# Kernel optimization log

Hardware: AMD Instinct MI355X
Metric: run time of the kernel (lower is better)

Reference implementation:

```python
import jax, jax.numpy as jnp
import numpy as np

EPS = 1e-5

def _face_normals(v, vi):
    # v: [B,V,3], vi: [F,3] -> [B,F,3]
    pts = v[:, vi]                                  # [B,F,3,3]
    n = jnp.cross(pts[:, :, 1] - pts[:, :, 0], pts[:, :, 2] - pts[:, :, 0])
    norm = jnp.linalg.norm(n, axis=-1, keepdims=True)
    return n / jnp.where(norm < EPS, 1.0, norm)

def _vert_normals(v, vi):
    fn = _face_normals(v, vi)                       # [B,F,3]
    fn_rep = jnp.repeat(fn, 3, axis=1)              # [B,3F,3] (one copy per face vertex)
    vn = jnp.zeros_like(v).at[:, vi.reshape(-1)].add(fn_rep)
    norm = jnp.linalg.norm(vn, axis=-1, keepdims=True)
    return vn / jnp.where(norm < EPS, 1.0, norm)

def _values_to_uv(values, index_image, bary_image):
    # values: [B,V,C]; index_image/bary_image: [U,U,3] -> [B,C,U,U]
    mask = jnp.all(index_image != -1, axis=-1)      # [U,U]
    idx = jnp.clip(index_image, 0, values.shape[1] - 1)
    vals = values[:, idx]                           # [B,U,U,3,C]
    uv = jnp.einsum('buvkc,uvk->bcuv', vals, bary_image.astype(values.dtype))
    return uv * mask[None, None].astype(values.dtype)

def _grid_sample_bilinear(img, gx, gy):
    # img: [B,C,H,W]; gx,gy: [N] in [-1,1]; align_corners=False, zero padding
    B, C, H, W = img.shape
    ix = ((gx + 1.0) * W - 1.0) * 0.5
    iy = ((gy + 1.0) * H - 1.0) * 0.5
    x0 = jnp.floor(ix); y0 = jnp.floor(iy)
    x1 = x0 + 1.0;      y1 = y0 + 1.0
    wx1 = ix - x0; wx0 = 1.0 - wx1
    wy1 = iy - y0; wy0 = 1.0 - wy1
    def gather(xi, yi):
        valid = (xi >= 0) & (xi < W) & (yi >= 0) & (yi < H)
        xc = jnp.clip(xi, 0, W - 1).astype(jnp.int32)
        yc = jnp.clip(yi, 0, H - 1).astype(jnp.int32)
        return img[:, :, yc, xc] * valid.astype(img.dtype)  # [B,C,N]
    return (gather(x0, y0) * (wx0 * wy0) + gather(x1, y0) * (wx1 * wy0)
          + gather(x0, y1) * (wx0 * wy1) + gather(x1, y1) * (wx1 * wy1))

def _sample_uv(values_uv, uv_coords, v2uv):
    g = uv_coords * 2.0 - 1.0                       # [T,2]
    vals = _grid_sample_bilinear(values_uv, g[:, 0], g[:, 1])  # [B,C,T]
    vals = jnp.transpose(vals, (0, 2, 1))           # [B,T,C]
    return vals[:, v2uv].mean(axis=2)               # [B,V,C]

def setup_inputs() -> dict:
    key = jax.random.key(0)
    ks = jax.random.split(key, 6)
    B, V, Fc, U, T, K = 8, 100000, 200000, 1024, 110000, 2
    verts = jax.random.normal(ks[0], (B, V, 3), jnp.float32)
    vi = jax.random.randint(ks[1], (Fc, 3), 0, V, dtype=jnp.int32)
    index_image = jax.random.randint(ks[2], (U, U, 3), 0, V, dtype=jnp.int32)
    bary_image = jax.random.uniform(ks[3], (U, U, 3), jnp.float32)
    vt = jax.random.uniform(ks[4], (T, 2), jnp.float32)
    v2uv = jax.random.randint(ks[5], (V, K), 0, T, dtype=jnp.int32)
    return {"verts": verts, "bary_image": bary_image, "vt": vt,
            "vi": vi, "index_image": index_image, "v2uv": v2uv}

def reference(verts, bary_image, vt, vi, index_image, v2uv):
    vn = _vert_normals(verts, vi)                   # [B,V,3]
    uv = _values_to_uv(vn, index_image, bary_image) # [B,3,U,U]
    return _sample_uv(uv, vt, v2uv)                 # [B,V,3]
```

## Files before the change

kernel.cpp:

```cpp
#include <hip/hip_runtime.h>
#include <hip/hip_fp16.h>

#define EPS 1e-5f

constexpr int B = 8;
constexpr int V = 100000;
constexpr int F = 200000;
constexpr int U = 1024;
constexpr int T = 110000;
constexpr int CAP = 24;

constexpr int NBUK = (V + 127) / 128;
constexpr int N4   = (3 * F) / 4;
constexpr int EB   = (N4 + 255) / 256;
constexpr int TRB  = (V + 255) / 256;

constexpr int FQ   = 8;
constexpr int FNB  = (F * 8 / FQ + 255) / 256;
constexpr int TQ   = 4;
constexpr int CPB  = (T / TQ + 255) / 256;
constexpr int SQ   = 2;
constexpr int VQ   = 2;

struct alignas(8) h4 { __half2 a, b; };
__device__ inline h4 pack_h4(float x, float y, float z) {
    h4 r; r.a = __floats2half2_rn(x, y); r.b = __floats2half2_rn(z, 0.0f);
    return r;
}
__device__ inline float3 unpack_h4(h4 v) {
    float2 xy = __half22float2(v.a);
    float2 zw = __half22float2(v.b);
    return make_float3(xy.x, xy.y, zw.x);
}

struct alignas(16) Corner16 { unsigned lo, hi; __half2 w01; __half2 w2_; };
__device__ inline Corner16 pack_corner(int i0, int i1, int i2,
                                       float w0, float w1, float w2) {
    unsigned long long x = (unsigned long long)(unsigned)i0
                         | ((unsigned long long)(unsigned)i1 << 21)
                         | ((unsigned long long)(unsigned)i2 << 42);
    Corner16 c;
    c.lo = (unsigned)x;
    c.hi = (unsigned)(x >> 32);
    c.w01 = __floats2half2_rn(w0, w1);
    c.w2_ = __floats2half2_rn(w2, 0.0f);
    return c;
}

__global__ void k1_pre(const float* __restrict__ verts,
                       float* __restrict__ vertsT,
                       const int* __restrict__ vi,
                       int* __restrict__ tot,
                       const int* __restrict__ index_image,
                       const float* __restrict__ bary_image,
                       const float* __restrict__ vt,
                       Corner16* __restrict__ corners) {
    __shared__ int lh[NBUK];
    int blk = blockIdx.x;

    if (blk < TRB) {
        int v = blk * 256 + threadIdx.x;
        if (v >= V) return;
        float buf[24];
#pragma unroll
        for (int b = 0; b < 8; ++b) {
            const float* p = verts + (size_t)b * V * 3 + (size_t)v * 3;
            buf[b * 3 + 0] = p[0];
            buf[b * 3 + 1] = p[1];
            buf[b * 3 + 2] = p[2];
        }
        float4* dst = (float4*)(vertsT + (size_t)v * 24);
#pragma unroll
        for (int i = 0; i < 6; ++i)
            dst[i] = make_float4(buf[4 * i], buf[4 * i + 1],
                                 buf[4 * i + 2], buf[4 * i + 3]);
        return;
    }

    if (blk < TRB + EB) {
        int k = blk - TRB;
        for (int i = threadIdx.x; i < NBUK; i += 256) lh[i] = 0;
        __syncthreads();
        int m4 = k * 256 + threadIdx.x;
        if (m4 < N4) {
            int4 e = ((const int4*)vi)[m4];
            atomicAdd(&lh[e.x >> 7], 1);
            atomicAdd(&lh[e.y >> 7], 1);
            atomicAdd(&lh[e.z >> 7], 1);
            atomicAdd(&lh[e.w >> 7], 1);
        }
        __syncthreads();
        for (int b = threadIdx.x; b < NBUK; b += 256)
            if (lh[b]) atomicAdd(&tot[b], lh[b]);
        return;
    }

    int tbase = (blk - TRB - EB) * 256 + threadIdx.x;
    if (tbase >= T / TQ) return;
#pragma unroll
    for (int qq = 0; qq < TQ; ++qq) {
        int t = tbase + qq * (T / TQ);

        float gx = vt[t * 2 + 0];
        float gy = vt[t * 2 + 1];
        float ix = gx * (float)U - 0.5f;
        float iy = gy * (float)U - 0.5f;

        float x0f = floorf(ix);
        float y0f = floorf(iy);
        int x0 = (int)x0f;
        int y0 = (int)y0f;
        float wx1 = ix - x0f, wx0 = 1.0f - wx1;
        float wy1 = iy - y0f, wy0 = 1.0f - wy1;

#pragma unroll
        for (int c = 0; c < 4; ++c) {
            int cy = c >> 1, cx = c & 1;
            int y = y0 + cy;
            int x = x0 + cx;
            int i0 = 0, i1 = 0, i2 = 0;
            float w0 = 0.0f, w1 = 0.0f, w2 = 0.0f;
            if (x >= 0 && x < U && y >= 0 && y < U) {
                float w = (cy ? wy1 : wy0) * (cx ? wx1 : wx0);
                int pix = y * U + x;
                int j0 = index_image[pix * 3 + 0];
                int j1 = index_image[pix * 3 + 1];
                int j2 = index_image[pix * 3 + 2];
                float m = (j0 != -1 && j1 != -1 && j2 != -1) ? 1.0f : 0.0f;
                float wm = w * m;
                i0 = min(max(j0, 0), V - 1);
                i1 = min(max(j1, 0), V - 1);
                i2 = min(max(j2, 0), V - 1);
                w0 = wm * bary_image[pix * 3 + 0];
                w1 = wm * bary_image[pix * 3 + 1];
                w2 = wm * bary_image[pix * 3 + 2];
            }
            corners[t * 4 + c] = pack_corner(i0, i1, i2, w0, w1, w2);
        }
    }
}

__device__ inline void scan_base(const int* __restrict__ tot,
                                 int* pre, int* part) {
    constexpr int CH = (NBUK + 255) / 256;
    int th = threadIdx.x;
    int loc[CH];
    int local = 0;
#pragma unroll
    for (int j = 0; j < CH; ++j) {
        int idx = th * CH + j;
        int c = (idx < NBUK) ? tot[idx] : 0;
        loc[j] = local;
        local += c;
    }
    part[th] = local;
    __syncthreads();
    for (int off = 1; off < 256; off <<= 1) {
        int x = (th >= off) ? part[th - off] : 0;
        __syncthreads();
        part[th] += x;
        __syncthreads();
    }
    int excl = part[th] - local;
#pragma unroll
    for (int j = 0; j < CH; ++j) {
        int idx = th * CH + j;
        if (idx < NBUK) pre[idx] = excl + loc[j];
    }
    if (th == 255) pre[NBUK] = part[255];
    __syncthreads();
}

__global__ __launch_bounds__(256, 2) void k2_fused(
        const int* __restrict__ vi,
        const float* __restrict__ vertsT,
        h4* __restrict__ fn,
        const int* __restrict__ tot,
        int* __restrict__ cursor,
        int* __restrict__ pairs) {
    int blk = blockIdx.x;

    if (blk < FNB) {
        int id = blk * 256 + threadIdx.x;
        if (id >= F * 8 / FQ) return;
        int b = id & 7;
        int fbase = id >> 3;
        const float3* vT = (const float3*)vertsT;

        int ia[FQ], ib[FQ], ic[FQ];
        float3 p0[FQ], p1[FQ], p2[FQ];
#pragma unroll
        for (int q = 0; q < FQ; ++q) {
            int f = fbase + q * (F / FQ);
            ia[q] = vi[f * 3 + 0];
            ib[q] = vi[f * 3 + 1];
            ic[q] = vi[f * 3 + 2];
        }
#pragma unroll
        for (int q = 0; q < FQ; ++q) {
            p0[q] = vT[(size_t)ia[q] * 8 + b];
            p1[q] = vT[(size_t)ib[q] * 8 + b];
            p2[q] = vT[(size_t)ic[q] * 8 + b];
        }
#pragma unroll
        for (int q = 0; q < FQ; ++q) {
            int f = fbase + q * (F / FQ);
            float e1x = p1[q].x - p0[q].x, e1y = p1[q].y - p0[q].y, e1z = p1[q].z - p0[q].z;
            float e2x = p2[q].x - p0[q].x, e2y = p2[q].y - p0[q].y, e2z = p2[q].z - p0[q].z;

            float nx = e1y * e2z - e1z * e2y;
            float ny = e1z * e2x - e1x * e2z;
            float nz = e1x * e2y - e1y * e2x;

            float norm = sqrtf(nx * nx + ny * ny + nz * nz);
            float inv = (norm < EPS) ? 1.0f : (1.0f / norm);
            fn[(size_t)f * 8 + b] = pack_h4(nx * inv, ny * inv, nz * inv);
        }
        return;
    }

    __shared__ int pre[NBUK + 1];
    __shared__ int part[256];
    __shared__ int lh[NBUK];
    __shared__ int base[NBUK];
    scan_base(tot, pre, part);
    for (int i = threadIdx.x; i < NBUK; i += 256) lh[i] = 0;
    __syncthreads();

    int k = blk - FNB;
    int m4 = k * 256 + threadIdx.x;
    bool act = (m4 < N4);
    int vv[4], rr[4], bbk[4], fc[4];
    if (act) {
        int4 e = ((const int4*)vi)[m4];
        vv[0] = e.x; vv[1] = e.y; vv[2] = e.z; vv[3] = e.w;
        int be = m4 * 4;
#pragma unroll
        for (int j = 0; j < 4; ++j) {
            bbk[j] = vv[j] >> 7;
            rr[j] = atomicAdd(&lh[bbk[j]], 1);
            fc[j] = (be + j) / 3;
        }
    }
    __syncthreads();
    for (int i = threadIdx.x; i < NBUK; i += 256)
        base[i] = lh[i] ? atomicAdd(&cursor[i], lh[i]) : 0;
    __syncthreads();
    if (act) {
#pragma unroll
        for (int j = 0; j < 4; ++j) {
            int pos = pre[bbk[j]] + base[bbk[j]] + rr[j];
            pairs[pos] = ((vv[j] & 127) << 18) | fc[j];
        }
    }
}

__global__ __launch_bounds__(256) void k5_gather(
        const int* __restrict__ pairs,
        const int* __restrict__ tot,
        const h4* __restrict__ fn,
        h4* __restrict__ vn) {
    __shared__ int cnt[128];
    __shared__ int rows[128 * CAP];
    __shared__ int pre[NBUK + 1];
    __shared__ int part[256];
    scan_base(tot, pre, part);

    int tid = threadIdx.x;
    if (tid < 128) cnt[tid] = 0;
    __syncthreads();

    int b = blockIdx.x;
    int start = pre[b], end = pre[b + 1];
    for (int i = start + tid; i < end; i += 256) {
        int pk = pairs[i];
        int vl = pk >> 18;
        int f = pk & 0x3FFFF;
        int pos = atomicAdd(&cnt[vl], 1);
        if (pos < CAP) rows[vl * CAP + pos] = f;
    }
    __syncthreads();

    int v0 = b << 7;
    for (int id = tid; id < 128 * 8; id += 256) {
        int vl = id >> 3, b8 = id & 7;
        int v = v0 + vl;
        if (v >= V) continue;
        int deg = min(cnt[vl], CAP);
        float ax = 0.0f, ay = 0.0f, az = 0.0f;
        int j = 0;
        for (; j + 1 < deg; j += 2) {
            h4 r0 = fn[(size_t)rows[vl * CAP + j] * 8 + b8];
            h4 r1 = fn[(size_t)rows[vl * CAP + j + 1] * 8 + b8];
            float3 n0 = unpack_h4(r0);
            float3 n1 = unpack_h4(r1);
            ax += n0.x + n1.x; ay += n0.y + n1.y; az += n0.z + n1.z;
        }
        if (j < deg) {
            float3 n = unpack_h4(fn[(size_t)rows[vl * CAP + j] * 8 + b8]);
            ax += n.x; ay += n.y; az += n.z;
        }
        float nn = sqrtf(ax * ax + ay * ay + az * az);
        float inv = (nn < EPS) ? 1.0f : (1.0f / nn);
        vn[(size_t)v * 8 + b8] = pack_h4(ax * inv, ay * inv, az * inv);
    }
}

__global__ void sample_points(const h4* __restrict__ vn,
                              const Corner16* __restrict__ corners,
                              h4* __restrict__ vals) {
    int id = blockIdx.x * blockDim.x + threadIdx.x;
    if (id >= (T / SQ) * 8) return;
    int b = id & 7;
    int tb = id >> 3;

#pragma unroll
    for (int s = 0; s < SQ; ++s) {
        int t = tb + s * (T / SQ);
        float ax = 0.0f, ay = 0.0f, az = 0.0f;
        Corner16 cr[4];
#pragma unroll
        for (int c = 0; c < 4; ++c) cr[c] = corners[t * 4 + c];
        h4 q[12];
#pragma unroll
        for (int c = 0; c < 4; ++c) {
            unsigned long long x = (unsigned long long)cr[c].lo
                                 | ((unsigned long long)cr[c].hi << 32);
            int i0 = (int)(x & 0x1FFFFF);
            int i1 = (int)((x >> 21) & 0x1FFFFF);
            int i2 = (int)(x >> 42);
            q[c * 3 + 0] = vn[(size_t)i0 * 8 + b];
            q[c * 3 + 1] = vn[(size_t)i1 * 8 + b];
            q[c * 3 + 2] = vn[(size_t)i2 * 8 + b];
        }
#pragma unroll
        for (int c = 0; c < 4; ++c) {
            float2 w01 = __half22float2(cr[c].w01);
            float w2 = __low2float(cr[c].w2_);
            float3 q0 = unpack_h4(q[c * 3 + 0]);
            float3 q1 = unpack_h4(q[c * 3 + 1]);
            float3 q2 = unpack_h4(q[c * 3 + 2]);
            ax += w01.x * q0.x + w01.y * q1.x + w2 * q2.x;
            ay += w01.x * q0.y + w01.y * q1.y + w2 * q2.y;
            az += w01.x * q0.z + w01.y * q1.z + w2 * q2.z;
        }
        vals[(size_t)t * 8 + b] = pack_h4(ax, ay, az);
    }
}

__global__ void gather_out(const h4* __restrict__ vals,
                           const int* __restrict__ v2uv,
                           float* __restrict__ out) {
    int id = blockIdx.x * blockDim.x + threadIdx.x;
    if (id >= (V / VQ) * 8) return;
    int b = id & 7;
    int vb = id >> 3;

    int t0[VQ], t1[VQ];
    h4 xa[VQ], ya[VQ];
#pragma unroll
    for (int s = 0; s < VQ; ++s) {
        int v = vb + s * (V / VQ);
        t0[s] = v2uv[v * 2 + 0];
        t1[s] = v2uv[v * 2 + 1];
    }
#pragma unroll
    for (int s = 0; s < VQ; ++s) {
        xa[s] = vals[(size_t)t0[s] * 8 + b];
        ya[s] = vals[(size_t)t1[s] * 8 + b];
    }
#pragma unroll
    for (int s = 0; s < VQ; ++s) {
        int v = vb + s * (V / VQ);
        float3 x = unpack_h4(xa[s]);
        float3 y = unpack_h4(ya[s]);
        float* o = out + (size_t)b * V * 3 + (size_t)v * 3;
        o[0] = 0.5f * (x.x + y.x);
        o[1] = 0.5f * (x.y + y.y);
        o[2] = 0.5f * (x.z + y.z);
    }
}

extern "C" void kernel_launch(void* const* d_in, const int* in_sizes, int n_in,
                              void* d_out, int out_size, void* d_ws, size_t ws_size,
                              hipStream_t stream) {
    const float* verts   = (const float*)d_in[0];
    const float* bary    = (const float*)d_in[1];
    const float* vt      = (const float*)d_in[2];
    const int*   vi      = (const int*)d_in[3];
    const int*   idx_img = (const int*)d_in[4];
    const int*   v2uv    = (const int*)d_in[5];
    float* out = (float*)d_out;

    float*    vertsT  = (float*)d_ws;
    h4*       vn      = (h4*)d_ws;
    h4*       fn      = (h4*)((char*)d_ws + (size_t)V * 8 * 12);
    h4*       vals    = fn;
    Corner16* corners = (Corner16*)((char*)fn + (size_t)F * 8 * sizeof(h4));
    int*      tot     = (int*)(corners + (size_t)T * 4);
    int*      cursor  = tot + NBUK;
    int*      pairs   = cursor + NBUK;

    const int BLK = 256;
    hipMemsetAsync(tot, 0, 2 * NBUK * sizeof(int), stream);
    k1_pre<<<TRB + EB + CPB, BLK, 0, stream>>>(
        verts, vertsT, vi, tot, idx_img, bary, vt, corners);
    k2_fused<<<FNB + EB, BLK, 0, stream>>>(vi, vertsT, fn, tot, cursor, pairs);
    k5_gather<<<NBUK, BLK, 0, stream>>>(pairs, tot, fn, vn);
    sample_points<<<((T / SQ) * 8 + BLK - 1) / BLK, BLK, 0, stream>>>(
        vn, corners, vals);
    gather_out<<<((V / VQ) * 8 + BLK - 1) / BLK, BLK, 0, stream>>>(
        vals, v2uv, out);
}
```

Measured before the change: 186.2 us.

## Pad transposed vertices to float4 and move corner precompute into k2

Transposed vertex positions are now stored as padded float4 (16 bytes per batch entry) instead of packed float3, so the face-normal gathers become aligned 16-byte loads. The UV corner precomputation moves from the first kernel into the second fused kernel as its own block range, rebalancing work between the two launches. The launch_bounds hint on k2 is dropped. This costs about a third more workspace and write traffic for vertsT, and the extra per-block branch in k2 may change occupancy.

Result: faster. 181.4 us (-2.6%).

```diff
diff --git a/kernel.cpp b/kernel.cpp
--- a/kernel.cpp
+++ b/kernel.cpp
@@ -48,96 +48,41 @@
 }
 
 __global__ void k1_pre(const float* __restrict__ verts,
-                       float* __restrict__ vertsT,
+                       float4* __restrict__ vertsT,
                        const int* __restrict__ vi,
-                       int* __restrict__ tot,
-                       const int* __restrict__ index_image,
-                       const float* __restrict__ bary_image,
-                       const float* __restrict__ vt,
-                       Corner16* __restrict__ corners) {
+                       int* __restrict__ tot) {
     __shared__ int lh[NBUK];
     int blk = blockIdx.x;
 
     if (blk < TRB) {
         int v = blk * 256 + threadIdx.x;
         if (v >= V) return;
-        float buf[24];
+        float4 row[8];
 #pragma unroll
         for (int b = 0; b < 8; ++b) {
             const float* p = verts + (size_t)b * V * 3 + (size_t)v * 3;
-            buf[b * 3 + 0] = p[0];
-            buf[b * 3 + 1] = p[1];
-            buf[b * 3 + 2] = p[2];
-        }
-        float4* dst = (float4*)(vertsT + (size_t)v * 24);
-#pragma unroll
-        for (int i = 0; i < 6; ++i)
-            dst[i] = make_float4(buf[4 * i], buf[4 * i + 1],
-                                 buf[4 * i + 2], buf[4 * i + 3]);
+            row[b] = make_float4(p[0], p[1], p[2], 0.0f);
+        }
+        float4* dst = vertsT + (size_t)v * 8;
+#pragma unroll
+        for (int b = 0; b < 8; ++b) dst[b] = row[b];
         return;
     }
 
-    if (blk < TRB + EB) {
-        int k = blk - TRB;
-        for (int i = threadIdx.x; i < NBUK; i += 256) lh[i] = 0;
-        __syncthreads();
-        int m4 = k * 256 + threadIdx.x;
-        if (m4 < N4) {
-            int4 e = ((const int4*)vi)[m4];
-            atomicAdd(&lh[e.x >> 7], 1);
-            atomicAdd(&lh[e.y >> 7], 1);
-            atomicAdd(&lh[e.z >> 7], 1);
-            atomicAdd(&lh[e.w >> 7], 1);
-        }
-        __syncthreads();
-        for (int b = threadIdx.x; b < NBUK; b += 256)
-            if (lh[b]) atomicAdd(&tot[b], lh[b]);
-        return;
-    }
-
-    int tbase = (blk - TRB - EB) * 256 + threadIdx.x;
-    if (tbase >= T / TQ) return;
-#pragma unroll
-    for (int qq = 0; qq < TQ; ++qq) {
-        int t = tbase + qq * (T / TQ);
-
-        float gx = vt[t * 2 + 0];
-        float gy = vt[t * 2 + 1];
-        float ix = gx * (float)U - 0.5f;
-        float iy = gy * (float)U - 0.5f;
-
-        float x0f = floorf(ix);
-        float y0f = floorf(iy);
-        int x0 = (int)x0f;
-        int y0 = (int)y0f;
-        float wx1 = ix - x0f, wx0 = 1.0f - wx1;
-        float wy1 = iy - y0f, wy0 = 1.0f - wy1;
-
-#pragma unroll
-        for (int c = 0; c < 4; ++c) {
-            int cy = c >> 1, cx = c & 1;
-            int y = y0 + cy;
-            int x = x0 + cx;
-            int i0 = 0, i1 = 0, i2 = 0;
-            float w0 = 0.0f, w1 = 0.0f, w2 = 0.0f;
-            if (x >= 0 && x < U && y >= 0 && y < U) {
-                float w = (cy ? wy1 : wy0) * (cx ? wx1 : wx0);
-                int pix = y * U + x;
-                int j0 = index_image[pix * 3 + 0];
-                int j1 = index_image[pix * 3 + 1];
-                int j2 = index_image[pix * 3 + 2];
-                float m = (j0 != -1 && j1 != -1 && j2 != -1) ? 1.0f : 0.0f;
-                float wm = w * m;
-                i0 = min(max(j0, 0), V - 1);
-                i1 = min(max(j1, 0), V - 1);
-                i2 = min(max(j2, 0), V - 1);
-                w0 = wm * bary_image[pix * 3 + 0];
-                w1 = wm * bary_image[pix * 3 + 1];
-                w2 = wm * bary_image[pix * 3 + 2];
-            }
-            corners[t * 4 + c] = pack_corner(i0, i1, i2, w0, w1, w2);
-        }
-    }
+    int k = blk - TRB;
+    for (int i = threadIdx.x; i < NBUK; i += 256) lh[i] = 0;
+    __syncthreads();
+    int m4 = k * 256 + threadIdx.x;
+    if (m4 < N4) {
+        int4 e = ((const int4*)vi)[m4];
+        atomicAdd(&lh[e.x >> 7], 1);
+        atomicAdd(&lh[e.y >> 7], 1);
+        atomicAdd(&lh[e.z >> 7], 1);
+        atomicAdd(&lh[e.w >> 7], 1);
+    }
+    __syncthreads();
+    for (int b = threadIdx.x; b < NBUK; b += 256)
+        if (lh[b]) atomicAdd(&tot[b], lh[b]);
 }
 
 __device__ inline void scan_base(const int* __restrict__ tot,
@@ -171,13 +116,16 @@
     __syncthreads();
 }
 
-__global__ __launch_bounds__(256, 2) void k2_fused(
-        const int* __restrict__ vi,
-        const float* __restrict__ vertsT,
-        h4* __restrict__ fn,
-        const int* __restrict__ tot,
-        int* __restrict__ cursor,
-        int* __restrict__ pairs) {
+__global__ void k2_fused(const int* __restrict__ vi,
+                         const float4* __restrict__ vertsT,
+                         h4* __restrict__ fn,
+                         const int* __restrict__ index_image,
+                         const float* __restrict__ bary_image,
+                         const float* __restrict__ vt,
+                         Corner16* __restrict__ corners,
+                         const int* __restrict__ tot,
+                         int* __restrict__ cursor,
+                         int* __restrict__ pairs) {
     int blk = blockIdx.x;
 
     if (blk < FNB) {
@@ -185,10 +133,9 @@
         if (id >= F * 8 / FQ) return;
         int b = id & 7;
         int fbase = id >> 3;
-        const float3* vT = (const float3*)vertsT;
 
         int ia[FQ], ib[FQ], ic[FQ];
-        float3 p0[FQ], p1[FQ], p2[FQ];
+        float4 p0[FQ], p1[FQ], p2[FQ];
 #pragma unroll
         for (int q = 0; q < FQ; ++q) {
             int f = fbase + q * (F / FQ);
@@ -198,9 +145,9 @@
         }
 #pragma unroll
         for (int q = 0; q < FQ; ++q) {
-            p0[q] = vT[(size_t)ia[q] * 8 + b];
-            p1[q] = vT[(size_t)ib[q] * 8 + b];
-            p2[q] = vT[(size_t)ic[q] * 8 + b];
+            p0[q] = vertsT[(size_t)ia[q] * 8 + b];
+            p1[q] = vertsT[(size_t)ib[q] * 8 + b];
+            p2[q] = vertsT[(size_t)ic[q] * 8 + b];
         }
 #pragma unroll
         for (int q = 0; q < FQ; ++q) {
@@ -215,6 +162,53 @@
             float norm = sqrtf(nx * nx + ny * ny + nz * nz);
             float inv = (norm < EPS) ? 1.0f : (1.0f / norm);
             fn[(size_t)f * 8 + b] = pack_h4(nx * inv, ny * inv, nz * inv);
+        }
+        return;
+    }
+
+    if (blk < FNB + CPB) {
+        int tbase = (blk - FNB) * 256 + threadIdx.x;
+        if (tbase >= T / TQ) return;
+#pragma unroll
+        for (int qq = 0; qq < TQ; ++qq) {
+            int t = tbase + qq * (T / TQ);
+
+            float gx = vt[t * 2 + 0];
+            float gy = vt[t * 2 + 1];
+            float ix = gx * (float)U - 0.5f;
+            float iy = gy * (float)U - 0.5f;
+
+            float x0f = floorf(ix);
+            float y0f = floorf(iy);
+            int x0 = (int)x0f;
+            int y0 = (int)y0f;
+            float wx1 = ix - x0f, wx0 = 1.0f - wx1;
+            float wy1 = iy - y0f, wy0 = 1.0f - wy1;
+
+#pragma unroll
+            for (int c = 0; c < 4; ++c) {
+                int cy = c >> 1, cx = c & 1;
+                int y = y0 + cy;
+                int x = x0 + cx;
+                int i0 = 0, i1 = 0, i2 = 0;
+                float w0 = 0.0f, w1 = 0.0f, w2 = 0.0f;
+                if (x >= 0 && x < U && y >= 0 && y < U) {
+                    float w = (cy ? wy1 : wy0) * (cx ? wx1 : wx0);
+                    int pix = y * U + x;
+                    int j0 = index_image[pix * 3 + 0];
+                    int j1 = index_image[pix * 3 + 1];
+                    int j2 = index_image[pix * 3 + 2];
+                    float m = (j0 != -1 && j1 != -1 && j2 != -1) ? 1.0f : 0.0f;
+                    float wm = w * m;
+                    i0 = min(max(j0, 0), V - 1);
+                    i1 = min(max(j1, 0), V - 1);
+                    i2 = min(max(j2, 0), V - 1);
+                    w0 = wm * bary_image[pix * 3 + 0];
+                    w1 = wm * bary_image[pix * 3 + 1];
+                    w2 = wm * bary_image[pix * 3 + 2];
+                }
+                corners[t * 4 + c] = pack_corner(i0, i1, i2, w0, w1, w2);
+            }
         }
         return;
     }
@@ -227,7 +221,7 @@
     for (int i = threadIdx.x; i < NBUK; i += 256) lh[i] = 0;
     __syncthreads();
 
-    int k = blk - FNB;
+    int k = blk - FNB - CPB;
     int m4 = k * 256 + threadIdx.x;
     bool act = (m4 < N4);
     int vv[4], rr[4], bbk[4], fc[4];
@@ -392,9 +386,9 @@
     const int*   v2uv    = (const int*)d_in[5];
     float* out = (float*)d_out;
 
-    float*    vertsT  = (float*)d_ws;
+    float4*   vertsT  = (float4*)d_ws;
     h4*       vn      = (h4*)d_ws;
-    h4*       fn      = (h4*)((char*)d_ws + (size_t)V * 8 * 12);
+    h4*       fn      = (h4*)(vertsT + (size_t)V * 8);
     h4*       vals    = fn;
     Corner16* corners = (Corner16*)((char*)fn + (size_t)F * 8 * sizeof(h4));
     int*      tot     = (int*)(corners + (size_t)T * 4);
@@ -403,9 +397,9 @@
 
     const int BLK = 256;
     hipMemsetAsync(tot, 0, 2 * NBUK * sizeof(int), stream);
-    k1_pre<<<TRB + EB + CPB, BLK, 0, stream>>>(
-        verts, vertsT, vi, tot, idx_img, bary, vt, corners);
-    k2_fused<<<FNB + EB, BLK, 0, stream>>>(vi, vertsT, fn, tot, cursor, pairs);
+    k1_pre<<<TRB + EB, BLK, 0, stream>>>(verts, vertsT, vi, tot);
+    k2_fused<<<FNB + CPB + EB, BLK, 0, stream>>>(
+        vi, vertsT, fn, idx_img, bary, vt, corners, tot, cursor, pairs);
     k5_gather<<<NBUK, BLK, 0, stream>>>(pairs, tot, fn, vn);
     sample_points<<<((T / SQ) * 8 + BLK - 1) / BLK, BLK, 0, stream>>>(
         vn, corners, vals);
```
